# Kernel optimization log

Hardware: AMD Instinct MI355X
Metric: run time of the kernel (lower is better)

The kernel has to match this reference:

```python
import math
import jax, jax.numpy as jnp
import numpy as np

D_MODEL = 128
D_STATE = 16
EXPAND = 2
D_INNER = EXPAND * D_MODEL
DT_RANK = math.ceil(D_MODEL / 16)  # 8
B, H, W = 2, 64, 64


def _wavefront_scan(dAT, dAL, BX):
    # 2D selective-scan recurrence:
    #   h[i,j] = dAT[i,j]*h[i-1,j] + dAL[i,j]*h[i,j-1] + BX[i,j]
    # all tensors [B,H,W,E,N]. Rows processed sequentially (lax.scan);
    # within a row the 1D linear recurrence over W uses associative_scan.
    def combine(c1, c2):
        a1, b1 = c1
        a2, b2 = c2
        return a1 * a2, a2 * b1 + b2

    def row_step(h_prev, row):  # h_prev: [B,W,E,N]
        dat, dal, bx = row
        b = dat * h_prev + bx
        _, h_row = jax.lax.associative_scan(combine, (dal, b), axis=1)
        return h_row, h_row

    rows = (jnp.moveaxis(dAT, 1, 0), jnp.moveaxis(dAL, 1, 0), jnp.moveaxis(BX, 1, 0))
    h0 = jnp.zeros_like(dAT[:, 0])
    _, hs = jax.lax.scan(row_step, h0, rows)
    return jnp.moveaxis(hs, 0, 1)  # [B,H,W,E,N]


def setup_inputs() -> dict:
    key = jax.random.key(0)
    ks = jax.random.split(key, 8)
    s = 0.02
    dt_min, dt_max, dt_floor = 1e-3, 1e-1, 1e-4
    dt = jnp.exp(jax.random.uniform(ks[0], (D_INNER,)) * (math.log(dt_max) - math.log(dt_min)) + math.log(dt_min))
    dt = jnp.clip(dt, dt_floor, None)
    inv_dt = dt + jnp.log(-jnp.expm1(-dt))
    std = DT_RANK ** -0.5
    A_log = jnp.log(jnp.tile(jnp.arange(1, D_STATE + 1, dtype=jnp.float32), (D_INNER, 1)))
    return {
        "x": jax.random.normal(ks[1], (B, H, W, D_MODEL), jnp.float32),
        "in_proj_w": jax.random.normal(ks[2], (D_INNER, D_MODEL), jnp.float32) * s,
        "in_proj_b": jnp.zeros((D_INNER,), jnp.float32),
        "x_proj_w": jax.random.normal(ks[3], (2 * DT_RANK + 2 * D_STATE, D_INNER), jnp.float32) * s,
        "x_proj_b": jnp.zeros((2 * DT_RANK + 2 * D_STATE,), jnp.float32),
        "dtT_w": jax.random.uniform(ks[4], (D_INNER, DT_RANK), jnp.float32, -std, std),
        "dtT_b": inv_dt,
        "dtL_w": jax.random.uniform(ks[5], (D_INNER, DT_RANK), jnp.float32, -std, std),
        "dtL_b": inv_dt,
        "AT_log": A_log,
        "AL_log": A_log,
        "D": jnp.ones((D_INNER,), jnp.float32),
        "out_w": jax.random.normal(ks[6], (D_MODEL, D_INNER), jnp.float32) * s,
        "out_b": jnp.zeros((D_MODEL,), jnp.float32),
    }


def reference(x, in_proj_w, in_proj_b, x_proj_w, x_proj_b, dtT_w, dtT_b, dtL_w, dtL_b, AT_log, AL_log, D, out_w, out_b):
    # in_proj + GELU (torch nn.GELU default = exact erf form)
    u = jax.nn.gelu(x @ in_proj_w.T + in_proj_b, approximate=False)  # [B,H,W,E]
    AT = -jnp.exp(AT_log)  # [E,N]
    AL = -jnp.exp(AL_log)
    dbc = u @ x_proj_w.T + x_proj_b
    dT, dL, Bm, Cm = jnp.split(dbc, [DT_RANK, 2 * DT_RANK, 2 * DT_RANK + D_STATE], axis=-1)
    deltaT = jax.nn.softplus(dT @ dtT_w.T + dtT_b)  # [B,H,W,E]
    deltaL = jax.nn.softplus(dL @ dtL_w.T + dtL_b)
    dAT = jnp.exp(deltaT[..., None] * AT)  # [B,H,W,E,N]
    dAL = jnp.exp(deltaL[..., None] * AL)
    # BXT + BXL fused: (deltaT + deltaL) * B * x
    BX = (deltaT + deltaL)[..., None] * Bm[..., None, :] * u[..., None]
    hs = _wavefront_scan(dAT, dAL, BX)  # [B,H,W,E,N]
    y = jnp.einsum('bhwen,bhwn->bhwe', hs, Cm) + u * D
    y = jax.nn.gelu(y, approximate=False)
    return y @ out_w.T + out_b
```

## Files before the change

kernel.cpp:

```cpp
#include <hip/hip_runtime.h>
#include <hip/hip_bf16.h>
#include <math.h>

#define BB 2
#define HH 64
#define WW 64
#define DM 128
#define EE 256
#define NN 16
#define RR 8
#define HW (HH*WW)
#define CH 16
#define NCH (HH/CH)

typedef __attribute__((ext_vector_type(8))) short bf16x8;
typedef __attribute__((ext_vector_type(4))) float f32x4;

__device__ __forceinline__ float gelu_exact(float v) {
    const float c = 0.79788456080286535588f, a = 0.044715f;
    const float t2 = 2.f * c * fmaf(a * v * v, v, v);
    const float e = __expf(t2);
    const float th = 1.f - 2.f * __frcp_rn(e + 1.f);
    return 0.5f * v * (1.f + th);
}
__device__ __forceinline__ float softplus_f(float v) {
    const float z = __expf(-fabsf(v));
    return fmaxf(v, 0.f) + 0.69314718055994530942f * __log2f(1.f + z);
}

__device__ __forceinline__ short2 pk2(float lo, float hi) {
    __hip_bfloat162 h = __float22bfloat162_rn(make_float2(lo, hi));
    union { __hip_bfloat162 h2; short2 s2; } u;
    u.h2 = h;
    return u.s2;
}

template<int S>
__device__ __forceinline__ float dpp_shr0(float x) {
    return __int_as_float(__builtin_amdgcn_update_dpp(
        0, __float_as_int(x), 0x110 | S, 0xF, 0xF, false));
}

__global__ __launch_bounds__(256) void kprep(
    const float* __restrict__ ipw, const float* __restrict__ xpw,
    const float* __restrict__ ow,
    short* __restrict__ ipw_bf, short* __restrict__ xpw_bf,
    short* __restrict__ ow_bf)
{
    const int blk = blockIdx.x;
    const float* src;
    short* dst;
    size_t off;
    if (blk < 16)      { src = ipw; dst = ipw_bf; off = (size_t)blk * 2048; }
    else if (blk < 22) { src = xpw; dst = xpw_bf; off = (size_t)(blk - 16) * 2048; }
    else               { src = ow;  dst = ow_bf;  off = (size_t)(blk - 22) * 2048; }

    const size_t p = off + (size_t)threadIdx.x * 8;
    const float4 a = *(const float4*)(src + p);
    const float4 b = *(const float4*)(src + p + 4);
    const short2 s0 = pk2(a.x, a.y), s1 = pk2(a.z, a.w);
    const short2 s2 = pk2(b.x, b.y), s3 = pk2(b.z, b.w);
    bf16x8 r;
    r[0] = s0.x; r[1] = s0.y; r[2] = s1.x; r[3] = s1.y;
    r[4] = s2.x; r[5] = s2.y; r[6] = s3.x; r[7] = s3.y;
    *(bf16x8*)(dst + p) = r;
}

__global__ __launch_bounds__(512, 4) void k1_fused(
    const float* __restrict__ x,
    const short* __restrict__ ipw_bf, const float* __restrict__ ipb,
    const short* __restrict__ xpw_bf, const float* __restrict__ xpb,
    const float* __restrict__ dtTw, const float* __restrict__ dtTb,
    const float* __restrict__ dtLw, const float* __restrict__ dtLb,
    float* __restrict__ u_t, float* __restrict__ dT_t, float* __restrict__ dL_t,
    float* __restrict__ Bm_t, float* __restrict__ Cm_t)
{
    __shared__ short xT[16][136];
    __shared__ short usT[16][264];
    __shared__ float parts[8][3][16][16];
    __shared__ float dbcs[48][17];

    const int blk = blockIdx.x;
    const int jq = blk & 3;
    const int row = blk >> 2;
    const int b = row >> 6, i = row & 63;
    const int t = threadIdx.x;
    const int w = t >> 6;
    const int lane = t & 63;
    const int l16 = lane & 15, lq = lane >> 4;
    const int j0 = 16 * jq;

    {
        const int j = t >> 5, k = (t & 31) * 4;
        const float4 a = *(const float4*)(
            x + (size_t)row * (WW * DM) + (size_t)(j0 + j) * DM + k);
        *(short2*)&xT[j][k]     = pk2(a.x, a.y);
        *(short2*)&xT[j][k + 2] = pk2(a.z, a.w);
    }
    __syncthreads();

    f32x4 acc0 = {0.f, 0.f, 0.f, 0.f};
    f32x4 acc1 = {0.f, 0.f, 0.f, 0.f};

    #pragma unroll
    for (int ks = 0; ks < 4; ++ks) {
        const int k0 = ks * 32 + lq * 8;
        const bf16x8 bfrag = *(const bf16x8*)&xT[l16][k0];
        const int eb = 32 * w;
        const bf16x8 a0 = *(const bf16x8*)(ipw_bf + (size_t)(eb +  0 + l16) * DM + k0);
        acc0 = __builtin_amdgcn_mfma_f32_16x16x32_bf16(a0, bfrag, acc0, 0, 0, 0);
        const bf16x8 a1 = *(const bf16x8*)(ipw_bf + (size_t)(eb + 16 + l16) * DM + k0);
        acc1 = __builtin_amdgcn_mfma_f32_16x16x32_bf16(a1, bfrag, acc1, 0, 0, 0);
    }

    #pragma unroll
    for (int ti = 0; ti < 2; ++ti) {
        const f32x4 acc = (ti == 0) ? acc0 : acc1;
        const int e_b = 32 * w + 16 * ti + lq * 4;
        const int j = j0 + l16;
        float g[4];
        #pragma unroll
        for (int r = 0; r < 4; ++r) {
            const int e = e_b + r;
            g[r] = gelu_exact(acc[r] + ipb[e]);
            u_t[(((size_t)(b * EE + e) * HH + i) << 6) + j] = g[r];
        }
        *(short2*)&usT[l16][e_b]     = pk2(g[0], g[1]);
        *(short2*)&usT[l16][e_b + 2] = pk2(g[2], g[3]);
    }
    __syncthreads();

    {
        const int e0 = 32 * w + lq * 8;
        const bf16x8 bfrag = *(const bf16x8*)&usT[l16][e0];
        #pragma unroll
        for (int ct = 0; ct < 3; ++ct) {
            f32x4 acc = {0.f, 0.f, 0.f, 0.f};
            const bf16x8 afrag = *(const bf16x8*)(xpw_bf + (size_t)(ct * 16 + l16) * EE + e0);
            acc = __builtin_amdgcn_mfma_f32_16x16x32_bf16(afrag, bfrag, acc, 0, 0, 0);
            #pragma unroll
            for (int r = 0; r < 4; ++r)
                parts[w][ct][lq * 4 + r][l16] = acc[r];
        }
    }
    __syncthreads();

    for (int idx = t; idx < 48 * 16; idx += 512) {
        const int c = idx >> 4, jj = idx & 15;
        const int ct = c >> 4, cm = c & 15;
        float s = xpb[c];
        #pragma unroll
        for (int w2 = 0; w2 < 8; ++w2) s += parts[w2][ct][cm][jj];
        dbcs[c][jj] = s;
    }
    __syncthreads();

    if (t < 256) {
        const int n = t >> 4, jj = t & 15;
        Bm_t[(((size_t)(b * NN + n) * HH + i) << 6) + j0 + jj] = dbcs[16 + n][jj];
        Cm_t[(((size_t)(b * NN + n) * HH + i) << 6) + j0 + jj] = dbcs[32 + n][jj];
    }

    {
        const int eg2 = t >> 4, jj = t & 15;
        float dtv[8], dlv[8];
        #pragma unroll
        for (int r = 0; r < 8; ++r) { dtv[r] = dbcs[r][jj]; dlv[r] = dbcs[8 + r][jj]; }
        #pragma unroll 4
        for (int ee = 0; ee < 8; ++ee) {
            const int e = eg2 * 8 + ee;
            float sT = dtTb[e], sL = dtLb[e];
            #pragma unroll
            for (int r = 0; r < 8; ++r) {
                sT = fmaf(dtv[r], dtTw[e * RR + r], sT);
                sL = fmaf(dlv[r], dtLw[e * RR + r], sL);
            }
            dT_t[(((size_t)(b * EE + e) * HH + i) << 6) + j0 + jj] = softplus_f(sT);
            dL_t[(((size_t)(b * EE + e) * HH + i) << 6) + j0 + jj] = softplus_f(sL);
        }
    }
}

__device__ __forceinline__ void row_scan_g(
    float4 dT4, float4 dL4, float4 u4, float4 bm4, float4 cm4,
    float AT2, float AL2, float* h, int jj, float* g)
{
    const float dTv[4] = {dT4.x, dT4.y, dT4.z, dT4.w};
    const float dLv[4] = {dL4.x, dL4.y, dL4.z, dL4.w};
    const float uv[4]  = {u4.x,  u4.y,  u4.z,  u4.w};
    const float bmv[4] = {bm4.x, bm4.y, bm4.z, bm4.w};
    const float cmv[4] = {cm4.x, cm4.y, cm4.z, cm4.w};

    float cumA[4], cumB[4];
    {
        const float aT = exp2f(dTv[0] * AT2);
        cumA[0] = exp2f(dLv[0] * AL2);
        cumB[0] = fmaf(aT, h[0], (dTv[0] + dLv[0]) * bmv[0] * uv[0]);
    }
    #pragma unroll
    for (int k = 1; k < 4; ++k) {
        const float aT = exp2f(dTv[k] * AT2);
        const float aL = exp2f(dLv[k] * AL2);
        const float bk = fmaf(aT, h[k], (dTv[k] + dLv[k]) * bmv[k] * uv[k]);
        cumB[k] = fmaf(aL, cumB[k - 1], bk);
        cumA[k] = aL * cumA[k - 1];
    }

    float Ag = cumA[3], Bg = cumB[3];
    { const float uA = dpp_shr0<1>(Ag), uB = dpp_shr0<1>(Bg);
      Bg = fmaf(Ag, uB, Bg); Ag *= (jj >= 1) ? uA : 1.f; }
    { const float uA = dpp_shr0<2>(Ag), uB = dpp_shr0<2>(Bg);
      Bg = fmaf(Ag, uB, Bg); Ag *= (jj >= 2) ? uA : 1.f; }
    { const float uA = dpp_shr0<4>(Ag), uB = dpp_shr0<4>(Bg);
      Bg = fmaf(Ag, uB, Bg); Ag *= (jj >= 4) ? uA : 1.f; }
    { const float uB = dpp_shr0<8>(Bg);
      Bg = fmaf(Ag, uB, Bg); }
    const float pB = dpp_shr0<1>(Bg);

    #pragma unroll
    for (int k = 0; k < 4; ++k) {
        h[k] = fmaf(cumA[k], pB, cumB[k]);
        g[k] = h[k] * cmv[k];
    }
}

__global__ __launch_bounds__(256, 2) void k2a_scan(
    const float* __restrict__ u_t, const float* __restrict__ dT_t,
    const float* __restrict__ dL_t, const float* __restrict__ Bm_t,
    const float* __restrict__ Cm_t, const float* __restrict__ ATl,
    const float* __restrict__ ALl, const float* __restrict__ Dp,
    float* __restrict__ ys_t)
{
    __shared__ float sdT[2][CH][64];
    __shared__ float sdL[2][CH][64];
    __shared__ float su [2][CH][64];
    __shared__ float parts[8][NN][68];

    const int be = blockIdx.x;
    const int b = be >> 8, e = be & 255;
    const int t = threadIdx.x;
    const int w = __builtin_amdgcn_readfirstlane(t >> 6);
    const int lane = t & 63;
    const int c = lane >> 4, jj = lane & 15;
    const int n = w * 4 + c;

    const float LOG2E = 1.44269504088896340736f;
    const float AT2 = -__expf(ATl[e * NN + n]) * LOG2E;
    const float AL2 = -__expf(ALl[e * NN + n]) * LOG2E;
    const float De = Dp[e];

    const float* dTg = dT_t + ((size_t)be << 12);
    const float* dLg = dL_t + ((size_t)be << 12);
    const float* ug  = u_t  + ((size_t)be << 12);
    const float* bmp = Bm_t + ((size_t)(b * NN + n) << 12) + 4 * jj;
    const float* cmp = Cm_t + ((size_t)(b * NN + n) << 12) + 4 * jj;

    const int srow = t >> 4;
    const int scol = (t & 15) << 2;
    float* ysf = ys_t + ((size_t)be << 12);

    float4 ldT, ldL, lu;
    {
        const size_t off = ((size_t)srow << 6) + scol;
        ldT = *(const float4*)(dTg + off);
        ldL = *(const float4*)(dLg + off);
        lu  = *(const float4*)(ug  + off);
        *(float4*)&sdT[0][srow][scol] = ldT;
        *(float4*)&sdL[0][srow][scol] = ldL;
        *(float4*)&su [0][srow][scol] = lu;
    }
    __syncthreads();

    float4 bm4 = *(const float4*)(bmp);
    float4 cm4 = *(const float4*)(cmp);

    float h[4] = {0.f, 0.f, 0.f, 0.f};

    for (int ch = 0; ch < NCH; ++ch) {
        const int buf = ch & 1;

        if (ch + 1 < NCH) {
            const size_t off = ((size_t)((ch + 1) * CH + srow) << 6) + scol;
            ldT = *(const float4*)(dTg + off);
            ldL = *(const float4*)(dLg + off);
            lu  = *(const float4*)(ug  + off);
            __builtin_amdgcn_sched_barrier(0);
        }

        #pragma unroll
        for (int hf = 0; hf < 2; ++hf) {
            #pragma unroll
            for (int r8 = 0; r8 < 8; ++r8) {
                const int r = hf * 8 + r8;
                const int i = ch * CH + r;
                const int ipn = (i + 1 < HH) ? i + 1 : i;
                const float4 bm4n = *(const float4*)(bmp + (ipn << 6));
                const float4 cm4n = *(const float4*)(cmp + (ipn << 6));

                const float4 dT4 = *(const float4*)&sdT[buf][r][4 * jj];
                const float4 dL4 = *(const float4*)&sdL[buf][r][4 * jj];
                const float4 u4  = *(const float4*)&su [buf][r][4 * jj];

                float g[4];
                row_scan_g(dT4, dL4, u4, bm4, cm4, AT2, AL2, h, jj, g);
                *(float4*)&parts[r8][n][4 * jj] = make_float4(g[0], g[1], g[2], g[3]);

                bm4 = bm4n; cm4 = cm4n;
            }

            if (hf == 1 && ch + 1 < NCH) {
                *(float4*)&sdT[buf ^ 1][srow][scol] = ldT;
                *(float4*)&sdL[buf ^ 1][srow][scol] = ldL;
                *(float4*)&su [buf ^ 1][srow][scol] = lu;
            }
            __syncthreads();

            #pragma unroll
            for (int q = 0; q < 2; ++q) {
                const int idx = t + (q << 8);
                const int r8 = idx >> 6, fcol = idx & 63;
                float s = 0.f;
                #pragma unroll
                for (int c2 = 0; c2 < NN; ++c2) s += parts[r8][c2][fcol];
                const float uu = su[buf][hf * 8 + r8][fcol];
                const int i = ch * CH + hf * 8 + r8;
                ysf[(i << 6) + fcol] = gelu_exact(fmaf(uu, De, s));
            }
            __syncthreads();
        }
    }
}

__global__ __launch_bounds__(256) void k3_outproj(
    const float* __restrict__ ys_t,
    const short* __restrict__ ow_bf, const float* __restrict__ ob,
    float* __restrict__ out)
{
    __shared__ short ysT[16][264];

    const int blk = blockIdx.x;
    const int jq = blk & 3;
    const int row = blk >> 2;
    const int b = row >> 6, i = row & 63;
    const int t = threadIdx.x;
    const int w = t >> 6;
    const int lane = t & 63;
    const int l16 = lane & 15, lq = lane >> 4;
    const int j0 = 16 * jq;

    for (int idx = t; idx < EE * 8; idx += 256) {
        const int e = idx >> 3, jp = idx & 7;
        const float2 v = *(const float2*)(
            ys_t + (((size_t)(b * EE + e) * HH + i) << 6) + j0 + 2 * jp);
        const short2 s = pk2(v.x, v.y);
        ysT[2 * jp][e] = s.x;
        ysT[2 * jp + 1][e] = s.y;
    }
    __syncthreads();

    f32x4 acc0 = {0.f, 0.f, 0.f, 0.f};
    f32x4 acc1 = {0.f, 0.f, 0.f, 0.f};

    const int d0 = 32 * w;

    #pragma unroll
    for (int ks = 0; ks < 8; ++ks) {
        const int e0 = ks * 32 + lq * 8;
        const bf16x8 afrag = *(const bf16x8*)&ysT[l16][e0];

        const bf16x8 b0 = *(const bf16x8*)(ow_bf + (size_t)(d0 + l16) * EE + e0);
        acc0 = __builtin_amdgcn_mfma_f32_16x16x32_bf16(afrag, b0, acc0, 0, 0, 0);
        const bf16x8 b1 = *(const bf16x8*)(ow_bf + (size_t)(d0 + 16 + l16) * EE + e0);
        acc1 = __builtin_amdgcn_mfma_f32_16x16x32_bf16(afrag, b1, acc1, 0, 0, 0);
    }

    float* orow = out + (size_t)row * (WW * DM);
    #pragma unroll
    for (int r = 0; r < 4; ++r) {
        const int j = j0 + lq * 4 + r;
        orow[(size_t)j * DM + d0 + l16]      = acc0[r] + ob[d0 + l16];
        orow[(size_t)j * DM + d0 + 16 + l16] = acc1[r] + ob[d0 + 16 + l16];
    }
}

extern "C" void kernel_launch(void* const* d_in, const int* in_sizes, int n_in,
                              void* d_out, int out_size, void* d_ws, size_t ws_size,
                              hipStream_t stream) {
    const float* x    = (const float*)d_in[0];
    const float* ipw  = (const float*)d_in[1];
    const float* ipb  = (const float*)d_in[2];
    const float* xpw  = (const float*)d_in[3];
    const float* xpb  = (const float*)d_in[4];
    const float* dtTw = (const float*)d_in[5];
    const float* dtTb = (const float*)d_in[6];
    const float* dtLw = (const float*)d_in[7];
    const float* dtLb = (const float*)d_in[8];
    const float* ATl  = (const float*)d_in[9];
    const float* ALl  = (const float*)d_in[10];
    const float* Dp   = (const float*)d_in[11];
    const float* ow   = (const float*)d_in[12];
    const float* ob   = (const float*)d_in[13];
    float* out = (float*)d_out;

    float* ws    = (float*)d_ws;
    float* u_t   = ws;
    float* dT_t  = u_t  + (size_t)BB * EE * HW;
    float* dL_t  = dT_t + (size_t)BB * EE * HW;
    float* ys_t  = dL_t + (size_t)BB * EE * HW;
    float* Bm_t  = ys_t + (size_t)BB * EE * HW;
    float* Cm_t  = Bm_t + (size_t)BB * NN * HW;
    float* bfp   = Cm_t + (size_t)BB * NN * HW;
    short* ipw_bf = (short*)bfp;
    short* xpw_bf = ipw_bf + (size_t)EE * DM;
    short* ow_bf  = xpw_bf + (size_t)48 * EE;

    kprep<<<38, 256, 0, stream>>>(ipw, xpw, ow, ipw_bf, xpw_bf, ow_bf);
    k1_fused<<<BB * HH * 4, 512, 0, stream>>>(x, ipw_bf, ipb, xpw_bf, xpb,
                                              dtTw, dtTb, dtLw, dtLb,
                                              u_t, dT_t, dL_t, Bm_t, Cm_t);
    k2a_scan<<<BB * EE, 256, 0, stream>>>(u_t, dT_t, dL_t, Bm_t, Cm_t,
                                          ATl, ALl, Dp, ys_t);
    k3_outproj<<<BB * HH * 4, 256, 0, stream>>>(ys_t, ow_bf, ob, out);
}
```

Before: 70.04 us.

## Widen scan block to 512 threads with 32-lane row scan per state

```diff
diff --git a/kernel.cpp b/kernel.cpp
--- a/kernel.cpp
+++ b/kernel.cpp
@@ -39,6 +39,10 @@
 __device__ __forceinline__ float dpp_shr0(float x) {
     return __int_as_float(__builtin_amdgcn_update_dpp(
         0, __float_as_int(x), 0x110 | S, 0xF, 0xF, false));
+}
+__device__ __forceinline__ float dpp_bc15(float x) {
+    return __int_as_float(__builtin_amdgcn_update_dpp(
+        0, __float_as_int(x), 0x142, 0xA, 0xF, false));
 }
 
 __global__ __launch_bounds__(256) void kprep(
@@ -181,50 +185,7 @@
     }
 }
 
-__device__ __forceinline__ void row_scan_g(
-    float4 dT4, float4 dL4, float4 u4, float4 bm4, float4 cm4,
-    float AT2, float AL2, float* h, int jj, float* g)
-{
-    const float dTv[4] = {dT4.x, dT4.y, dT4.z, dT4.w};
-    const float dLv[4] = {dL4.x, dL4.y, dL4.z, dL4.w};
-    const float uv[4]  = {u4.x,  u4.y,  u4.z,  u4.w};
-    const float bmv[4] = {bm4.x, bm4.y, bm4.z, bm4.w};
-    const float cmv[4] = {cm4.x, cm4.y, cm4.z, cm4.w};
-
-    float cumA[4], cumB[4];
-    {
-        const float aT = exp2f(dTv[0] * AT2);
-        cumA[0] = exp2f(dLv[0] * AL2);
-        cumB[0] = fmaf(aT, h[0], (dTv[0] + dLv[0]) * bmv[0] * uv[0]);
-    }
-    #pragma unroll
-    for (int k = 1; k < 4; ++k) {
-        const float aT = exp2f(dTv[k] * AT2);
-        const float aL = exp2f(dLv[k] * AL2);
-        const float bk = fmaf(aT, h[k], (dTv[k] + dLv[k]) * bmv[k] * uv[k]);
-        cumB[k] = fmaf(aL, cumB[k - 1], bk);
-        cumA[k] = aL * cumA[k - 1];
-    }
-
-    float Ag = cumA[3], Bg = cumB[3];
-    { const float uA = dpp_shr0<1>(Ag), uB = dpp_shr0<1>(Bg);
-      Bg = fmaf(Ag, uB, Bg); Ag *= (jj >= 1) ? uA : 1.f; }
-    { const float uA = dpp_shr0<2>(Ag), uB = dpp_shr0<2>(Bg);
-      Bg = fmaf(Ag, uB, Bg); Ag *= (jj >= 2) ? uA : 1.f; }
-    { const float uA = dpp_shr0<4>(Ag), uB = dpp_shr0<4>(Bg);
-      Bg = fmaf(Ag, uB, Bg); Ag *= (jj >= 4) ? uA : 1.f; }
-    { const float uB = dpp_shr0<8>(Bg);
-      Bg = fmaf(Ag, uB, Bg); }
-    const float pB = dpp_shr0<1>(Bg);
-
-    #pragma unroll
-    for (int k = 0; k < 4; ++k) {
-        h[k] = fmaf(cumA[k], pB, cumB[k]);
-        g[k] = h[k] * cmv[k];
-    }
-}
-
-__global__ __launch_bounds__(256, 2) void k2a_scan(
+__global__ __launch_bounds__(512, 4) void k2a_scan(
     const float* __restrict__ u_t, const float* __restrict__ dT_t,
     const float* __restrict__ dL_t, const float* __restrict__ Bm_t,
     const float* __restrict__ Cm_t, const float* __restrict__ ATl,
@@ -241,8 +202,11 @@
     const int t = threadIdx.x;
     const int w = __builtin_amdgcn_readfirstlane(t >> 6);
     const int lane = t & 63;
-    const int c = lane >> 4, jj = lane & 15;
-    const int n = w * 4 + c;
+    const int half = lane >> 5;
+    const int l32 = lane & 31;
+    const int l16 = lane & 15;
+    const int rq = lane >> 4;
+    const int n = 2 * w + half;
 
     const float LOG2E = 1.44269504088896340736f;
     const float AT2 = -__expf(ATl[e * NN + n]) * LOG2E;
@@ -252,38 +216,45 @@
     const float* dTg = dT_t + ((size_t)be << 12);
     const float* dLg = dL_t + ((size_t)be << 12);
     const float* ug  = u_t  + ((size_t)be << 12);
-    const float* bmp = Bm_t + ((size_t)(b * NN + n) << 12) + 4 * jj;
-    const float* cmp = Cm_t + ((size_t)(b * NN + n) << 12) + 4 * jj;
-
-    const int srow = t >> 4;
-    const int scol = (t & 15) << 2;
+    const float* bmp = Bm_t + ((size_t)(b * NN + n) << 12) + 2 * l32;
+    const float* cmp = Cm_t + ((size_t)(b * NN + n) << 12) + 2 * l32;
     float* ysf = ys_t + ((size_t)be << 12);
+
+    const int slot = t & 255;
+    const int srow = slot >> 4;
+    const int scol = (slot & 15) << 2;
 
     float4 ldT, ldL, lu;
     {
         const size_t off = ((size_t)srow << 6) + scol;
-        ldT = *(const float4*)(dTg + off);
-        ldL = *(const float4*)(dLg + off);
-        lu  = *(const float4*)(ug  + off);
-        *(float4*)&sdT[0][srow][scol] = ldT;
-        *(float4*)&sdL[0][srow][scol] = ldL;
-        *(float4*)&su [0][srow][scol] = lu;
-    }
-    __syncthreads();
-
-    float4 bm4 = *(const float4*)(bmp);
-    float4 cm4 = *(const float4*)(cmp);
-
-    float h[4] = {0.f, 0.f, 0.f, 0.f};
+        if (t < 256) {
+            ldT = *(const float4*)(dTg + off);
+            lu  = *(const float4*)(ug  + off);
+            *(float4*)&sdT[0][srow][scol] = ldT;
+            *(float4*)&su [0][srow][scol] = lu;
+        } else {
+            ldL = *(const float4*)(dLg + off);
+            *(float4*)&sdL[0][srow][scol] = ldL;
+        }
+    }
+    __syncthreads();
+
+    float2 bm2 = *(const float2*)(bmp);
+    float2 cm2 = *(const float2*)(cmp);
+
+    float h0 = 0.f, h1 = 0.f;
 
     for (int ch = 0; ch < NCH; ++ch) {
         const int buf = ch & 1;
 
         if (ch + 1 < NCH) {
             const size_t off = ((size_t)((ch + 1) * CH + srow) << 6) + scol;
-            ldT = *(const float4*)(dTg + off);
-            ldL = *(const float4*)(dLg + off);
-            lu  = *(const float4*)(ug  + off);
+            if (t < 256) {
+                ldT = *(const float4*)(dTg + off);
+                lu  = *(const float4*)(ug  + off);
+            } else {
+                ldL = *(const float4*)(dLg + off);
+            }
             __builtin_amdgcn_sched_barrier(0);
         }
 
@@ -294,31 +265,64 @@
                 const int r = hf * 8 + r8;
                 const int i = ch * CH + r;
                 const int ipn = (i + 1 < HH) ? i + 1 : i;
-                const float4 bm4n = *(const float4*)(bmp + (ipn << 6));
-                const float4 cm4n = *(const float4*)(cmp + (ipn << 6));
-
-                const float4 dT4 = *(const float4*)&sdT[buf][r][4 * jj];
-                const float4 dL4 = *(const float4*)&sdL[buf][r][4 * jj];
-                const float4 u4  = *(const float4*)&su [buf][r][4 * jj];
-
-                float g[4];
-                row_scan_g(dT4, dL4, u4, bm4, cm4, AT2, AL2, h, jj, g);
-                *(float4*)&parts[r8][n][4 * jj] = make_float4(g[0], g[1], g[2], g[3]);
-
-                bm4 = bm4n; cm4 = cm4n;
+                const float2 bm2n = *(const float2*)(bmp + (ipn << 6));
+                const float2 cm2n = *(const float2*)(cmp + (ipn << 6));
+
+                const float2 dT2 = *(const float2*)&sdT[buf][r][2 * l32];
+                const float2 dL2 = *(const float2*)&sdL[buf][r][2 * l32];
+                const float2 u2  = *(const float2*)&su [buf][r][2 * l32];
+
+                const float aT0 = exp2f(dT2.x * AT2);
+                const float aT1 = exp2f(dT2.y * AT2);
+                const float aL0 = exp2f(dL2.x * AL2);
+                const float aL1 = exp2f(dL2.y * AL2);
+                const float b0 = fmaf(aT0, h0, (dT2.x + dL2.x) * bm2.x * u2.x);
+                const float b1 = fmaf(aT1, h1, (dT2.y + dL2.y) * bm2.y * u2.y);
+
+                const float cumA0 = aL0;
+                const float cumB0 = b0;
+                const float cumA1 = aL1 * aL0;
+                const float cumB1 = fmaf(aL1, b0, b1);
+
+                float Ag = cumA1, Bg = cumB1;
+                { const float uA = dpp_shr0<1>(Ag), uB = dpp_shr0<1>(Bg);
+                  Bg = fmaf(Ag, uB, Bg); Ag *= (l16 >= 1) ? uA : 1.f; }
+                { const float uA = dpp_shr0<2>(Ag), uB = dpp_shr0<2>(Bg);
+                  Bg = fmaf(Ag, uB, Bg); Ag *= (l16 >= 2) ? uA : 1.f; }
+                { const float uA = dpp_shr0<4>(Ag), uB = dpp_shr0<4>(Bg);
+                  Bg = fmaf(Ag, uB, Bg); Ag *= (l16 >= 4) ? uA : 1.f; }
+                { const float uA = dpp_shr0<8>(Bg), uB = dpp_shr0<8>(Bg);
+                  (void)uA; (void)uB; }
+                { const float uA = dpp_shr0<8>(Ag), uB = dpp_shr0<8>(Bg);
+                  Bg = fmaf(Ag, uB, Bg); Ag *= (l16 >= 8) ? uA : 1.f; }
+                { const float uA = dpp_bc15(Ag), uB = dpp_bc15(Bg);
+                  Bg = fmaf(Ag, uB, Bg); Ag *= (rq & 1) ? uA : 1.f; }
+
+                const float pSh = dpp_shr0<1>(Bg);
+                const float pBc = dpp_bc15(Bg);
+                const float pB = (l16 == 0) ? pBc : pSh;
+
+                h0 = fmaf(cumA0, pB, cumB0);
+                h1 = fmaf(cumA1, pB, cumB1);
+
+                *(float2*)&parts[r8][n][2 * l32] =
+                    make_float2(h0 * cm2.x, h1 * cm2.y);
+
+                bm2 = bm2n; cm2 = cm2n;
             }
 
             if (hf == 1 && ch + 1 < NCH) {
-                *(float4*)&sdT[buf ^ 1][srow][scol] = ldT;
-                *(float4*)&sdL[buf ^ 1][srow][scol] = ldL;
-                *(float4*)&su [buf ^ 1][srow][scol] = lu;
+                if (t < 256) {
+                    *(float4*)&sdT[buf ^ 1][srow][scol] = ldT;
+                    *(float4*)&su [buf ^ 1][srow][scol] = lu;
+                } else {
+                    *(float4*)&sdL[buf ^ 1][srow][scol] = ldL;
+                }
             }
             __syncthreads();
 
-            #pragma unroll
-            for (int q = 0; q < 2; ++q) {
-                const int idx = t + (q << 8);
-                const int r8 = idx >> 6, fcol = idx & 63;
+            {
+                const int r8 = t >> 6, fcol = t & 63;
                 float s = 0.f;
                 #pragma unroll
                 for (int c2 = 0; c2 < NN; ++c2) s += parts[r8][c2][fcol];
@@ -418,7 +422,7 @@
     k1_fused<<<BB * HH * 4, 512, 0, stream>>>(x, ipw_bf, ipb, xpw_bf, xpb,
                                               dtTw, dtTb, dtLw, dtLb,
                                               u_t, dT_t, dL_t, Bm_t, Cm_t);
-    k2a_scan<<<BB * EE, 256, 0, stream>>>(u_t, dT_t, dL_t, Bm_t, Cm_t,
+    k2a_scan<<<BB * EE, 512, 0, stream>>>(u_t, dT_t, dL_t, Bm_t, Cm_t,
                                           ATl, ALl, Dp, ys_t);
     k3_outproj<<<BB * HH * 4, 256, 0, stream>>>(ys_t, ow_bf, ob, out);
 }
```

New measurement: 75.37 us. 7.6% more time.
